# Performance work log

Hardware: AMD Instinct MI355X
Metric: run time of the kernel (lower is better)

## Reference

```python
import jax, jax.numpy as jnp
import numpy as np

B, N, T = 128, 64, 20
I_CNN, H, E, L, NCLS, V = 24, 128, 300, 256, 100, 96


def _coords():
    # make_coords(64): 8x8 grid, grid = [(i - W//2)/W, (j - W//2)/W]
    W = 8
    g = (np.arange(W) - W // 2) / W
    c = np.stack(np.meshgrid(g, g, indexing='ij'), -1).reshape(W * W, 2)
    return jnp.asarray(c, jnp.float32)


def _lstm_final_c(seq, lens, w_ih, w_hh, b_ih, b_hh):
    # seq: [B,T,E]; returns cell state at each sequence's true length (packed-LSTM semantics)
    Bd = seq.shape[0]
    mask = (jnp.arange(T)[None, :] < lens[:, None]).astype(seq.dtype)  # [B,T]

    def step(carry, inp):
        h, c = carry
        x_t, m = inp  # [B,E], [B,1]
        gates = x_t @ w_ih.T + b_ih + h @ w_hh.T + b_hh  # [B,4H], torch gate order i,f,g,o
        i_g, f_g, g_g, o_g = jnp.split(gates, 4, axis=-1)
        c_new = jax.nn.sigmoid(f_g) * c + jax.nn.sigmoid(i_g) * jnp.tanh(g_g)
        h_new = jax.nn.sigmoid(o_g) * jnp.tanh(c_new)
        c = m * c_new + (1.0 - m) * c
        h = m * h_new + (1.0 - m) * h
        return (h, c), None

    h0 = jnp.zeros((Bd, H), seq.dtype)
    (_, cT), _ = jax.lax.scan(step, (h0, h0), (seq.transpose(1, 0, 2), mask.T[:, :, None]))
    return cT


def _forward(box_feats, emb, w_ih, w_hh, b_ih, b_hh,
             g_w1, g_b1, g_w2, g_b2, g_w3, g_b3, g_w4, g_b4,
             f_w1, f_b1, f_w2, f_b2, f_w3, f_b3, q_feats, q_lens):
    tok = jnp.tanh(emb[q_feats])  # [B,T,E]
    q_rnn = _lstm_final_c(tok, q_lens, w_ih, w_hh, b_ih, b_hh)  # [B,H]
    coords = jnp.broadcast_to(_coords()[None], (B, N, 2))
    box = jnp.concatenate([box_feats, coords], -1)  # [B,N,26]
    D = box.shape[-1]
    b_i = jnp.broadcast_to(box[:, :, None, :], (B, N, N, D))
    b_j = jnp.broadcast_to(box[:, None, :, :], (B, N, N, D))
    qst = jnp.broadcast_to(q_rnn[:, None, None, :], (B, N, N, H))
    b_full = jnp.concatenate([b_i, b_j, qst], -1).reshape(B * N * N, 2 * D + H)  # [B*N*N,180]
    x = jax.nn.relu(b_full @ g_w1 + g_b1)
    x = jax.nn.relu(x @ g_w2 + g_b2)
    x = jax.nn.relu(x @ g_w3 + g_b3)
    x = jax.nn.relu(x @ g_w4 + g_b4)
    g_out = x.reshape(B, N * N, L).sum(1)  # [B,256]
    y = jax.nn.relu(g_out @ f_w1 + f_b1)
    y = jax.nn.relu(y @ f_w2 + f_b2)
    return y @ f_w3 + f_b3  # [B,NCLS]  (dropout is identity at inference)


def setup_inputs() -> dict:
    key = jax.random.key(0)
    ks = jax.random.split(key, 16)

    def w(k, shape, s=0.05):
        return jax.random.normal(k, shape, jnp.float32) * s

    Din = 2 * (I_CNN + 2) + H  # 180
    z = lambda n: jnp.zeros((n,), jnp.float32)
    return dict(
        box_feats=jax.random.normal(ks[0], (B, N, I_CNN), jnp.float32),
        emb=w(ks[1], (V, E), 0.1),
        w_ih=w(ks[2], (4 * H, E)), w_hh=w(ks[3], (4 * H, H)),
        b_ih=z(4 * H), b_hh=z(4 * H),
        g_w1=w(ks[4], (Din, L)), g_b1=z(L),
        g_w2=w(ks[5], (L, L)), g_b2=z(L),
        g_w3=w(ks[6], (L, L)), g_b3=z(L),
        g_w4=w(ks[7], (L, L)), g_b4=z(L),
        f_w1=w(ks[8], (L, L)), f_b1=z(L),
        f_w2=w(ks[9], (L, L)), f_b2=z(L),
        f_w3=w(ks[10], (L, NCLS)), f_b3=z(NCLS),
        q_feats=jax.random.randint(ks[11], (B, T), 0, V),
        q_lens=jax.random.randint(ks[12], (B,), 1, T + 1),
    )


def reference(box_feats, emb, w_ih, w_hh, b_ih, b_hh,
              g_w1, g_b1, g_w2, g_b2, g_w3, g_b3, g_w4, g_b4,
              f_w1, f_b1, f_w2, f_b2, f_w3, f_b3, q_feats, q_lens):
    return _forward(box_feats, emb, w_ih, w_hh, b_ih, b_hh,
                    g_w1, g_b1, g_w2, g_b2, g_w3, g_b3, g_w4, g_b4,
                    f_w1, f_b1, f_w2, f_b2, f_w3, f_b3, q_feats, q_lens)
```

## Files before the change

### kernel.cpp

```cpp
#include <hip/hip_runtime.h>
#include <hip/hip_bf16.h>

typedef unsigned int uint;
typedef unsigned short ushort;
typedef __attribute__((ext_vector_type(8))) short bf16x8;
typedef __attribute__((ext_vector_type(4))) float f32x4;

__device__ __forceinline__ float bf2f(ushort u) {
    return __uint_as_float(((uint)u) << 16);
}
__device__ __forceinline__ ushort f2bf(float f) {
    uint u = __float_as_uint(f);
    u += 0x7FFFu + ((u >> 16) & 1u);
    return (ushort)(u >> 16);
}
__device__ __forceinline__ uint cvtpk(float lo, float hi) {
    uint r;
    asm("v_cvt_pk_bf16_f32 %0, %1, %2" : "=v"(r) : "v"(lo), "v"(hi));
    return r;
}
__device__ __forceinline__ float sigm(float x) {
    return 1.0f / (1.0f + expf(-x));
}

__global__ __launch_bounds__(512) void kPW(
    const float* __restrict__ emb, const float* __restrict__ w_ih,
    const float* __restrict__ b_ih, float* __restrict__ P,
    const float* __restrict__ g_w2, const float* __restrict__ g_w3,
    const float* __restrict__ g_w4, ushort* __restrict__ Wst)
{
    int tid = threadIdx.x;
    if (blockIdx.x < 96) {
        __shared__ __align__(16) float te[300];
        int v = blockIdx.x;
        for (int k = tid; k < 300; k += 512) te[k] = tanhf(emb[v * 300 + k]);
        __syncthreads();
        int g = tid;
        float acc = b_ih[g];
        const float4* wr = (const float4*)(w_ih + g * 300);
        const float4* tv = (const float4*)te;
        for (int k = 0; k < 75; ++k) {
            float4 w4 = wr[k], t4 = tv[k];
            acc += w4.x * t4.x + w4.y * t4.y + w4.z * t4.z + w4.w * t4.w;
        }
        P[v * 512 + g] = acc;
    } else if (tid < 256) {
        int blk = blockIdx.x - 96;
        int li = blk >> 3, kc = blk & 7, col = tid;
        const float* W = (li == 0) ? g_w2 : (li == 1) ? g_w3 : g_w4;
        ushort* dst = Wst + li * 65536 + kc * 8192
                    + (col >> 4) * 512 + (col & 15) * 8;
        for (int kk = 0; kk < 32; ++kk)
            dst[(kk >> 3) * 128 + (kk & 7)] = f2bf(W[(kc * 32 + kk) * 256 + col]);
    }
}

#define WROW 132
__global__ __launch_bounds__(512) void kLA(
    const float* __restrict__ P, const float* __restrict__ w_hh,
    const float* __restrict__ b_hh, const float* __restrict__ g_w1,
    const float* __restrict__ g_b1, const int* __restrict__ q_feats,
    const int* __restrict__ q_lens, const float* __restrict__ box_feats,
    ushort* __restrict__ A1, ushort* __restrict__ A2)
{
    __shared__ __align__(16) ushort whh[512 * WROW];
    __shared__ __align__(16) float h[128];
    __shared__ __align__(16) float c[128];
    __shared__ float gates[512];
    __shared__ float wq2[2][256];
    __shared__ float box[64][26];
    int b = blockIdx.x, tid = threadIdx.x;
    if (tid < 128) { h[tid] = 0.f; c[tid] = 0.f; }
    for (int i = tid * 4; i < 65536; i += 2048) {
        int g = i >> 7, k = i & 127;
        float4 w4 = *(const float4*)&w_hh[i];
        uint2 o;
        o.x = cvtpk(w4.x, w4.y);
        o.y = cvtpk(w4.z, w4.w);
        *(uint2*)&whh[g * WROW + k] = o;
    }
    for (int idx = tid; idx < 64 * 26; idx += 512) {
        int n = idx / 26, d = idx - n * 26;
        float v;
        if (d < 24)       v = box_feats[(b * 64 + n) * 24 + d];
        else if (d == 24) v = ((n >> 3) - 4) * 0.125f;
        else              v = ((n & 7) - 4) * 0.125f;
        box[n][d] = v;
    }
    __syncthreads();
    int len = q_lens[b];
    const int g = tid;
    const ushort* wr = &whh[g * WROW];
    for (int t = 0; t < len; ++t) {
        int idx = q_feats[b * 20 + t];
        float acc = P[idx * 512 + g] + b_hh[g];
        #pragma unroll
        for (int k8 = 0; k8 < 16; ++k8) {
            uint2 wlo = *(const uint2*)&wr[k8 * 8];
            uint2 whi = *(const uint2*)&wr[k8 * 8 + 4];
            float4 h0 = *(const float4*)&h[k8 * 8];
            float4 h1 = *(const float4*)&h[k8 * 8 + 4];
            acc += bf2f((ushort)(wlo.x & 0xFFFFu)) * h0.x
                 + bf2f((ushort)(wlo.x >> 16))     * h0.y
                 + bf2f((ushort)(wlo.y & 0xFFFFu)) * h0.z
                 + bf2f((ushort)(wlo.y >> 16))     * h0.w
                 + bf2f((ushort)(whi.x & 0xFFFFu)) * h1.x
                 + bf2f((ushort)(whi.x >> 16))     * h1.y
                 + bf2f((ushort)(whi.y & 0xFFFFu)) * h1.z
                 + bf2f((ushort)(whi.y >> 16))     * h1.w;
        }
        gates[g] = acc;
        __syncthreads();
        if (tid < 128) {
            float ig = sigm(gates[tid]);
            float fg = sigm(gates[128 + tid]);
            float gg = tanhf(gates[256 + tid]);
            float og = sigm(gates[384 + tid]);
            float cn = fg * c[tid] + ig * gg;
            c[tid] = cn;
            h[tid] = og * tanhf(cn);
        }
        __syncthreads();
    }
    {
        int l = tid & 255, half = tid >> 8;
        float acc = (half == 0) ? g_b1[l] : 0.f;
        for (int k = 0; k < 64; ++k)
            acc += c[half * 64 + k] * g_w1[(52 + half * 64 + k) * 256 + l];
        wq2[half][l] = acc;
    }
    __syncthreads();
    {
        int l = tid & 255, n0 = tid >> 8;
        float w1a[26], w1b[26];
        #pragma unroll
        for (int d = 0; d < 26; ++d) {
            w1a[d] = g_w1[d * 256 + l];
            w1b[d] = g_w1[(26 + d) * 256 + l];
        }
        float wqv = wq2[0][l] + wq2[1][l];
        for (int n = n0; n < 64; n += 2) {
            float a1 = 0.f, a2 = wqv;
            #pragma unroll
            for (int d = 0; d < 26; ++d) {
                a1 += box[n][d] * w1a[d];
                a2 += box[n][d] * w1b[d];
            }
            A1[(b * 64 + n) * 256 + l] = f2bf(a1);
            A2[(b * 64 + n) * 256 + l] = f2bf(a2);
        }
    }
}

#define MFMA1(wa, xb, a) __builtin_amdgcn_mfma_f32_16x16x32_bf16(wa, xb, a, 0, 0, 0)

__global__ __launch_bounds__(512, 2) void kD(
    const ushort* __restrict__ A1, const ushort* __restrict__ A2,
    const ushort* __restrict__ Wst,
    const float* __restrict__ b2, const float* __restrict__ b3,
    const float* __restrict__ b4, float* __restrict__ partial)
{
    __shared__ __align__(16) ushort lds_x[256 * 256];

    const int tid = threadIdx.x;
    const int b = blockIdx.x >> 4, iblk = blockIdx.x & 15;
    const int lane = tid & 63, wv = tid >> 6;
    const int l15 = lane & 15, lg = lane >> 4;
    const int wrow0 = (wv & 1) * 128, col0 = (wv >> 1) * 64;

    const int l0 = (tid & 31) << 3;
    bf16x8 a1r[4];
    #pragma unroll
    for (int p = 0; p < 4; ++p)
        a1r[p] = *(const bf16x8*)&A1[(b * 64 + iblk * 4 + p) * 256 + l0];

    const ushort* A2b = A2 + b * 64 * 256;
    #pragma unroll
    for (int p8 = 0; p8 < 16; ++p8) {
        int row = p8 * 16 + (tid >> 5);
        int j = row & 63;
        uint4 v = *(const uint4*)(A2b + j * 256 + l0);
        bf16x8 a1v = a1r[p8 >> 2];
        uint vv[4] = {v.x, v.y, v.z, v.w}, ov[4];
        #pragma unroll
        for (int qq = 0; qq < 4; ++qq) {
            float f0 = bf2f((ushort)a1v[2 * qq])     + bf2f((ushort)(vv[qq] & 0xFFFFu));
            float f1 = bf2f((ushort)a1v[2 * qq + 1]) + bf2f((ushort)(vv[qq] >> 16));
            ov[qq] = cvtpk(fmaxf(f0, 0.f), fmaxf(f1, 0.f));
        }
        *(uint4*)&lds_x[row * 256 + (l0 ^ ((row & 7) << 3))] =
            make_uint4(ov[0], ov[1], ov[2], ov[3]);
    }
    __syncthreads();

    const char* wbase = (const char*)Wst + (col0 >> 4) * 1024 + lane * 16;

    #pragma unroll 1
    for (int li = 0; li < 3; ++li) {
        f32x4 acc[8][4];
        #pragma unroll
        for (int rt = 0; rt < 8; ++rt)
            #pragma unroll
            for (int ct = 0; ct < 4; ++ct)
                acc[rt][ct] = (f32x4){0.f, 0.f, 0.f, 0.f};

        #pragma unroll 1
        for (int kc = 0; kc < 8; ++kc) {
            const char* wp = wbase + li * 131072 + kc * 16384;
            bf16x8 wa0 = *(const bf16x8*)(wp);
            bf16x8 wa1 = *(const bf16x8*)(wp + 1024);
            bf16x8 wa2 = *(const bf16x8*)(wp + 2048);
            bf16x8 wa3 = *(const bf16x8*)(wp + 3072);
            bf16x8 xb[8];
            #pragma unroll
            for (int rt = 0; rt < 8; ++rt) {
                int row = wrow0 + rt * 16 + l15;
                xb[rt] = *(const bf16x8*)
                    &lds_x[row * 256 + ((kc * 32 + lg * 8) ^ ((row & 7) << 3))];
            }
            __builtin_amdgcn_s_setprio(1);
            #pragma unroll
            for (int rt = 0; rt < 8; ++rt) {
                acc[rt][0] = MFMA1(wa0, xb[rt], acc[rt][0]);
                acc[rt][1] = MFMA1(wa1, xb[rt], acc[rt][1]);
                acc[rt][2] = MFMA1(wa2, xb[rt], acc[rt][2]);
                acc[rt][3] = MFMA1(wa3, xb[rt], acc[rt][3]);
            }
            __builtin_amdgcn_s_setprio(0);
        }

        const float* bias = (li == 0) ? b2 : (li == 1) ? b3 : b4;
        f32x4 bv0 = *(const f32x4*)(bias + col0 + lg * 4);
        f32x4 bv1 = *(const f32x4*)(bias + col0 + 16 + lg * 4);
        f32x4 bv2 = *(const f32x4*)(bias + col0 + 32 + lg * 4);
        f32x4 bv3 = *(const f32x4*)(bias + col0 + 48 + lg * 4);

        if (li < 2) {
            __builtin_amdgcn_s_barrier();
            #pragma unroll
            for (int rt = 0; rt < 8; ++rt) {
                int row = wrow0 + rt * 16 + l15;
                int sw = (row & 7) << 3;
                #pragma unroll
                for (int ct = 0; ct < 4; ++ct) {
                    f32x4 a = acc[rt][ct];
                    f32x4 bv = (ct == 0) ? bv0 : (ct == 1) ? bv1 : (ct == 2) ? bv2 : bv3;
                    uint2 pk;
                    pk.x = cvtpk(fmaxf(a[0] + bv[0], 0.f), fmaxf(a[1] + bv[1], 0.f));
                    pk.y = cvtpk(fmaxf(a[2] + bv[2], 0.f), fmaxf(a[3] + bv[3], 0.f));
                    *(uint2*)&lds_x[row * 256 + ((col0 + ct * 16 + lg * 4) ^ sw)] = pk;
                }
            }
            asm volatile("s_waitcnt lgkmcnt(0)" ::: "memory");
            __builtin_amdgcn_sched_barrier(0);
            __builtin_amdgcn_s_barrier();
        } else {
            #pragma unroll
            for (int ct = 0; ct < 4; ++ct) {
                f32x4 bv = (ct == 0) ? bv0 : (ct == 1) ? bv1 : (ct == 2) ? bv2 : bv3;
                f32x4 s0 = {0.f, 0.f, 0.f, 0.f}, s1 = {0.f, 0.f, 0.f, 0.f};
                #pragma unroll
                for (int rt = 0; rt < 4; ++rt) {
                    f32x4 a = acc[rt][ct];
                    s0[0] += fmaxf(a[0] + bv[0], 0.f); s0[1] += fmaxf(a[1] + bv[1], 0.f);
                    s0[2] += fmaxf(a[2] + bv[2], 0.f); s0[3] += fmaxf(a[3] + bv[3], 0.f);
                }
                #pragma unroll
                for (int rt = 4; rt < 8; ++rt) {
                    f32x4 a = acc[rt][ct];
                    s1[0] += fmaxf(a[0] + bv[0], 0.f); s1[1] += fmaxf(a[1] + bv[1], 0.f);
                    s1[2] += fmaxf(a[2] + bv[2], 0.f); s1[3] += fmaxf(a[3] + bv[3], 0.f);
                }
                #pragma unroll
                for (int m = 1; m < 16; m <<= 1) {
                    #pragma unroll
                    for (int r = 0; r < 4; ++r) {
                        s0[r] += __shfl_xor(s0[r], m, 64);
                        s1[r] += __shfl_xor(s1[r], m, 64);
                    }
                }
                if (l15 == 0) {
                    int prow = b * 64 + iblk * 4 + (wv & 1) * 2;
                    float4 o0 = {s0[0], s0[1], s0[2], s0[3]};
                    float4 o1 = {s1[0], s1[1], s1[2], s1[3]};
                    *(float4*)&partial[(prow    ) * 256 + col0 + ct * 16 + lg * 4] = o0;
                    *(float4*)&partial[(prow + 1) * 256 + col0 + ct * 16 + lg * 4] = o1;
                }
            }
        }
    }
}

__global__ __launch_bounds__(256) void kRF(
    const float* __restrict__ partial,
    const float* __restrict__ f_w1, const float* __restrict__ f_b1,
    const float* __restrict__ f_w2, const float* __restrict__ f_b2,
    const float* __restrict__ f_w3, const float* __restrict__ f_b3,
    float* __restrict__ out)
{
    __shared__ float g[256], y1[256], y2[256];
    int b = blockIdx.x, t = threadIdx.x;
    {
        float s = 0.f;
        const float* pb = partial + b * 64 * 256 + t;
        #pragma unroll 8
        for (int i = 0; i < 64; ++i) s += pb[i * 256];
        g[t] = s;
    }
    __syncthreads();
    float acc = f_b1[t];
    for (int k = 0; k < 256; ++k) acc += g[k] * f_w1[k * 256 + t];
    y1[t] = fmaxf(acc, 0.f);
    __syncthreads();
    acc = f_b2[t];
    for (int k = 0; k < 256; ++k) acc += y1[k] * f_w2[k * 256 + t];
    y2[t] = fmaxf(acc, 0.f);
    __syncthreads();
    if (t < 100) {
        float o = f_b3[t];
        for (int k = 0; k < 256; ++k) o += y2[k] * f_w3[k * 100 + t];
        out[b * 100 + t] = o;
    }
}

extern "C" void kernel_launch(void* const* d_in, const int* in_sizes, int n_in,
                              void* d_out, int out_size, void* d_ws, size_t ws_size,
                              hipStream_t stream)
{
    const float* box_feats = (const float*)d_in[0];
    const float* emb   = (const float*)d_in[1];
    const float* w_ih  = (const float*)d_in[2];
    const float* w_hh  = (const float*)d_in[3];
    const float* b_ih  = (const float*)d_in[4];
    const float* b_hh  = (const float*)d_in[5];
    const float* g_w1  = (const float*)d_in[6];
    const float* g_b1  = (const float*)d_in[7];
    const float* g_w2  = (const float*)d_in[8];
    const float* g_b2  = (const float*)d_in[9];
    const float* g_w3  = (const float*)d_in[10];
    const float* g_b3  = (const float*)d_in[11];
    const float* g_w4  = (const float*)d_in[12];
    const float* g_b4  = (const float*)d_in[13];
    const float* f_w1  = (const float*)d_in[14];
    const float* f_b1  = (const float*)d_in[15];
    const float* f_w2  = (const float*)d_in[16];
    const float* f_b2  = (const float*)d_in[17];
    const float* f_w3  = (const float*)d_in[18];
    const float* f_b3  = (const float*)d_in[19];
    const int* q_feats = (const int*)d_in[20];
    const int* q_lens  = (const int*)d_in[21];
    float* out = (float*)d_out;

    char* ws = (char*)d_ws;
    float*  P    = (float*) (ws + 0);
    ushort* A1   = (ushort*)(ws + 196608);
    ushort* A2   = (ushort*)(ws + 4390912);
    ushort* Wst  = (ushort*)(ws + 8585216);
    float*  part = (float*) (ws + 8978432);

    hipLaunchKernelGGL(kPW, dim3(120),  dim3(512), 0, stream,
                       emb, w_ih, b_ih, P, g_w2, g_w3, g_w4, Wst);
    hipLaunchKernelGGL(kLA, dim3(128),  dim3(512), 0, stream,
                       P, w_hh, b_hh, g_w1, g_b1, q_feats, q_lens, box_feats, A1, A2);
    hipLaunchKernelGGL(kD,  dim3(2048), dim3(512), 0, stream,
                       A1, A2, Wst, g_b2, g_b3, g_b4, part);
    hipLaunchKernelGGL(kRF, dim3(128),  dim3(256), 0, stream,
                       part, f_w1, f_b1, f_w2, f_b2, f_w3, f_b3, out);
}
```

Measured before the change: 288.6 us.

## Halve per-block row tile in MLP kernel to raise occupancy

Each kD block now handles 128 pair rows (2 i values) instead of 256, halving the LDS buffer to 64 KB and the per-wave accumulator tile to 4x4, while launching twice as many blocks. Waves are rearranged into 2 row groups by 4 column groups, and launch bounds request 4 blocks per CU. The aim is more resident waves to hide latency. The cost is that each weight fragment loaded from global memory is reused across half as many rows, so weight traffic per unit of work doubles.

```diff
diff --git a/kernel.cpp b/kernel.cpp
--- a/kernel.cpp
+++ b/kernel.cpp
@@ -154,33 +154,34 @@
 
 #define MFMA1(wa, xb, a) __builtin_amdgcn_mfma_f32_16x16x32_bf16(wa, xb, a, 0, 0, 0)
 
-__global__ __launch_bounds__(512, 2) void kD(
+__global__ __launch_bounds__(512, 4) void kD(
     const ushort* __restrict__ A1, const ushort* __restrict__ A2,
     const ushort* __restrict__ Wst,
     const float* __restrict__ b2, const float* __restrict__ b3,
     const float* __restrict__ b4, float* __restrict__ partial)
 {
-    __shared__ __align__(16) ushort lds_x[256 * 256];
+    __shared__ __align__(16) ushort lds_x[128 * 256];
 
     const int tid = threadIdx.x;
-    const int b = blockIdx.x >> 4, iblk = blockIdx.x & 15;
+    const int b = blockIdx.x >> 5, iblk = blockIdx.x & 31;
     const int lane = tid & 63, wv = tid >> 6;
     const int l15 = lane & 15, lg = lane >> 4;
-    const int wrow0 = (wv & 1) * 128, col0 = (wv >> 1) * 64;
+    const int rg = wv >> 2, cg = wv & 3;
+    const int row0 = rg * 64, col0 = cg * 64;
 
     const int l0 = (tid & 31) << 3;
-    bf16x8 a1r[4];
+    bf16x8 a1r[2];
     #pragma unroll
-    for (int p = 0; p < 4; ++p)
-        a1r[p] = *(const bf16x8*)&A1[(b * 64 + iblk * 4 + p) * 256 + l0];
+    for (int p = 0; p < 2; ++p)
+        a1r[p] = *(const bf16x8*)&A1[(b * 64 + iblk * 2 + p) * 256 + l0];
 
     const ushort* A2b = A2 + b * 64 * 256;
     #pragma unroll
-    for (int p8 = 0; p8 < 16; ++p8) {
-        int row = p8 * 16 + (tid >> 5);
+    for (int it = 0; it < 8; ++it) {
+        int row = it * 16 + (tid >> 5);
         int j = row & 63;
         uint4 v = *(const uint4*)(A2b + j * 256 + l0);
-        bf16x8 a1v = a1r[p8 >> 2];
+        bf16x8 a1v = a1r[it >> 2];
         uint vv[4] = {v.x, v.y, v.z, v.w}, ov[4];
         #pragma unroll
         for (int qq = 0; qq < 4; ++qq) {
@@ -197,9 +198,9 @@
 
     #pragma unroll 1
     for (int li = 0; li < 3; ++li) {
-        f32x4 acc[8][4];
+        f32x4 acc[4][4];
         #pragma unroll
-        for (int rt = 0; rt < 8; ++rt)
+        for (int rt = 0; rt < 4; ++rt)
             #pragma unroll
             for (int ct = 0; ct < 4; ++ct)
                 acc[rt][ct] = (f32x4){0.f, 0.f, 0.f, 0.f};
@@ -211,16 +212,16 @@
             bf16x8 wa1 = *(const bf16x8*)(wp + 1024);
             bf16x8 wa2 = *(const bf16x8*)(wp + 2048);
             bf16x8 wa3 = *(const bf16x8*)(wp + 3072);
-            bf16x8 xb[8];
-            #pragma unroll
-            for (int rt = 0; rt < 8; ++rt) {
-                int row = wrow0 + rt * 16 + l15;
+            bf16x8 xb[4];
+            #pragma unroll
+            for (int rt = 0; rt < 4; ++rt) {
+                int row = row0 + rt * 16 + l15;
                 xb[rt] = *(const bf16x8*)
                     &lds_x[row * 256 + ((kc * 32 + lg * 8) ^ ((row & 7) << 3))];
             }
             __builtin_amdgcn_s_setprio(1);
             #pragma unroll
-            for (int rt = 0; rt < 8; ++rt) {
+            for (int rt = 0; rt < 4; ++rt) {
                 acc[rt][0] = MFMA1(wa0, xb[rt], acc[rt][0]);
                 acc[rt][1] = MFMA1(wa1, xb[rt], acc[rt][1]);
                 acc[rt][2] = MFMA1(wa2, xb[rt], acc[rt][2]);
@@ -238,8 +239,8 @@
         if (li < 2) {
             __builtin_amdgcn_s_barrier();
             #pragma unroll
-            for (int rt = 0; rt < 8; ++rt) {
-                int row = wrow0 + rt * 16 + l15;
+            for (int rt = 0; rt < 4; ++rt) {
+                int row = row0 + rt * 16 + l15;
                 int sw = (row & 7) << 3;
                 #pragma unroll
                 for (int ct = 0; ct < 4; ++ct) {
@@ -258,33 +259,24 @@
             #pragma unroll
             for (int ct = 0; ct < 4; ++ct) {
                 f32x4 bv = (ct == 0) ? bv0 : (ct == 1) ? bv1 : (ct == 2) ? bv2 : bv3;
-                f32x4 s0 = {0.f, 0.f, 0.f, 0.f}, s1 = {0.f, 0.f, 0.f, 0.f};
+                f32x4 s = {0.f, 0.f, 0.f, 0.f};
                 #pragma unroll
                 for (int rt = 0; rt < 4; ++rt) {
                     f32x4 a = acc[rt][ct];
-                    s0[0] += fmaxf(a[0] + bv[0], 0.f); s0[1] += fmaxf(a[1] + bv[1], 0.f);
-                    s0[2] += fmaxf(a[2] + bv[2], 0.f); s0[3] += fmaxf(a[3] + bv[3], 0.f);
-                }
-                #pragma unroll
-                for (int rt = 4; rt < 8; ++rt) {
-                    f32x4 a = acc[rt][ct];
-                    s1[0] += fmaxf(a[0] + bv[0], 0.f); s1[1] += fmaxf(a[1] + bv[1], 0.f);
-                    s1[2] += fmaxf(a[2] + bv[2], 0.f); s1[3] += fmaxf(a[3] + bv[3], 0.f);
+                    s[0] += fmaxf(a[0] + bv[0], 0.f);
+                    s[1] += fmaxf(a[1] + bv[1], 0.f);
+                    s[2] += fmaxf(a[2] + bv[2], 0.f);
+                    s[3] += fmaxf(a[3] + bv[3], 0.f);
                 }
                 #pragma unroll
                 for (int m = 1; m < 16; m <<= 1) {
                     #pragma unroll
-                    for (int r = 0; r < 4; ++r) {
-                        s0[r] += __shfl_xor(s0[r], m, 64);
-                        s1[r] += __shfl_xor(s1[r], m, 64);
-                    }
+                    for (int r = 0; r < 4; ++r) s[r] += __shfl_xor(s[r], m, 64);
                 }
                 if (l15 == 0) {
-                    int prow = b * 64 + iblk * 4 + (wv & 1) * 2;
-                    float4 o0 = {s0[0], s0[1], s0[2], s0[3]};
-                    float4 o1 = {s1[0], s1[1], s1[2], s1[3]};
-                    *(float4*)&partial[(prow    ) * 256 + col0 + ct * 16 + lg * 4] = o0;
-                    *(float4*)&partial[(prow + 1) * 256 + col0 + ct * 16 + lg * 4] = o1;
+                    int prow = b * 64 + iblk * 2 + rg;
+                    float4 o = {s[0], s[1], s[2], s[3]};
+                    *(float4*)&partial[prow * 256 + col0 + ct * 16 + lg * 4] = o;
                 }
             }
         }
@@ -362,7 +354,7 @@
                        emb, w_ih, b_ih, P, g_w2, g_w3, g_w4, Wst);
     hipLaunchKernelGGL(kLA, dim3(128),  dim3(512), 0, stream,
                        P, w_hh, b_hh, g_w1, g_b1, q_feats, q_lens, box_feats, A1, A2);
-    hipLaunchKernelGGL(kD,  dim3(2048), dim3(512), 0, stream,
+    hipLaunchKernelGGL(kD,  dim3(4096), dim3(512), 0, stream,
                        A1, A2, Wst, g_b2, g_b3, g_b4, part);
     hipLaunchKernelGGL(kRF, dim3(128),  dim3(256), 0, stream,
                        part, f_w1, f_b1, f_w2, f_b2, f_w3, f_b3, out);
```

After: 285.0 us (median of 2 runs). No clear change (-1.2%).
